# Kernel optimization log

Measured on AMD Instinct MI355X. Metric: run time of the kernel, lower is better.

Reference implementation:

```python
import jax, jax.numpy as jnp
import numpy as np

N_NODES = 100000


def gcn_conv(x, src, dst, W, b):
    # PyG GCNConv: add self-loops, symmetric norm D^-1/2 (A+I) D^-1/2, then linear.
    n = x.shape[0]
    xw = x @ W  # [N, out]
    deg = jax.ops.segment_sum(jnp.ones_like(dst, dtype=xw.dtype), dst, num_segments=n)
    dinv = jnp.where(deg > 0, jax.lax.rsqrt(deg), 0.0)
    norm = dinv[src] * dinv[dst]  # [E_total]
    out = jax.ops.segment_sum(norm[:, None] * xw[src], dst, num_segments=n)
    return out + b


def setup_inputs() -> dict:
    key = jax.random.key(0)
    k1, k2, k3, k4, k5, k6 = jax.random.split(key, 6)
    d = 64
    E = 1600000
    x = jax.random.normal(k1, (N_NODES, d), dtype=jnp.float32)
    edge_index = jax.random.randint(k2, (2, E), 0, N_NODES, dtype=jnp.int64)
    s = 1.0 / np.sqrt(d)
    W1 = jax.random.normal(k3, (d, d), dtype=jnp.float32) * s
    b1 = jax.random.normal(k4, (d,), dtype=jnp.float32) * 0.01
    W2 = jax.random.normal(k5, (d, d), dtype=jnp.float32) * s
    b2 = jax.random.normal(k6, (d,), dtype=jnp.float32) * 0.01
    return {"x": x, "edge_index": edge_index, "W1": W1, "b1": b1, "W2": W2, "b2": b2}


def reference(x, edge_index, W1, b1, W2, b2):
    n = x.shape[0]
    loops = jnp.arange(n, dtype=edge_index.dtype)
    src = jnp.concatenate([edge_index[0], loops])
    dst = jnp.concatenate([edge_index[1], loops])
    out = jax.nn.relu(gcn_conv(x, src, dst, W1, b1))
    out = gcn_conv(out, src, dst, W2, b2)
    return jax.nn.relu(out + x)
```

## Files before the change

kernel.cpp:

```cpp
#include <hip/hip_runtime.h>

constexpr int BIN_CHUNK = 2048;
constexpr int BK_SHIFT  = 8;
constexpr int BK_NODES  = 1 << BK_SHIFT;
constexpr int NBMAX     = 512;
constexpr int CAP       = 5120;

typedef short bf16x8 __attribute__((ext_vector_type(8)));
typedef float f32x4 __attribute__((ext_vector_type(4)));

static __device__ __forceinline__ float4 mkf4(float x, float y, float z, float w) {
  float4 r; r.x = x; r.y = y; r.z = z; r.w = w; return r;
}

static __device__ __forceinline__ unsigned short bf16rne(float f) {
  unsigned u = __float_as_uint(f);
  u = (u + 0x7fffu + ((u >> 16) & 1u)) >> 16;
  return (unsigned short)u;
}
static __device__ __forceinline__ unsigned pack_bf16(float a, float b) {
  return (unsigned)bf16rne(a) | ((unsigned)bf16rne(b) << 16);
}
static __device__ __forceinline__ float blo(unsigned v) { return __uint_as_float(v << 16); }
static __device__ __forceinline__ float bhi(unsigned v) { return __uint_as_float(v & 0xffff0000u); }


__global__ void k_zero(int* __restrict__ p) { p[threadIdx.x] = 0; }


__global__ __launch_bounds__(256) void k_bin(const int* __restrict__ src,
                                             const int* __restrict__ dst,
                                             int* __restrict__ bcur,
                                             int* __restrict__ binned, int E) {
  __shared__ int lh[4][NBMAX];
  __shared__ int cbase[4][NBMAX];
  const int tid = threadIdx.x, wv = tid >> 6, lane = tid & 63;
  for (int i = lane; i < NBMAX; i += 64) lh[wv][i] = 0;
  __syncthreads();

  const int e0 = blockIdx.x * BIN_CHUNK;
  const int e1 = min(e0 + BIN_CHUNK, E);
  const int q  = BIN_CHUNK / 4;
  const int we0 = min(e0 + wv * q, e1);
  const int we1 = min(we0 + q, e1);
  const bool vec = (we1 - we0 == q) &&
                   (((((size_t)(dst + we0)) | ((size_t)(src + we0))) & 15) == 0);

  if (vec) {
    const int4* __restrict__ d4 = (const int4*)(dst + we0);
#pragma unroll
    for (int j = 0; j < 2; ++j) {
      int4 d = d4[lane + j * 64];
      atomicAdd(&lh[wv][d.x >> BK_SHIFT], 1);
      atomicAdd(&lh[wv][d.y >> BK_SHIFT], 1);
      atomicAdd(&lh[wv][d.z >> BK_SHIFT], 1);
      atomicAdd(&lh[wv][d.w >> BK_SHIFT], 1);
    }
  } else {
    for (int e = we0 + lane; e < we1; e += 64)
      atomicAdd(&lh[wv][dst[e] >> BK_SHIFT], 1);
  }
  __syncthreads();

  for (int b = tid; b < NBMAX; b += 256) {
    int c0 = lh[0][b], c1 = lh[1][b], c2 = lh[2][b], c3 = lh[3][b];
    int tot = c0 + c1 + c2 + c3;
    int base = tot ? atomicAdd(bcur + b, tot) : 0;
    cbase[0][b] = base;
    cbase[1][b] = base + c0;
    cbase[2][b] = base + c0 + c1;
    cbase[3][b] = base + c0 + c1 + c2;
    lh[0][b] = 0; lh[1][b] = 0; lh[2][b] = 0; lh[3][b] = 0;
  }
  __syncthreads();

  if (vec) {
    const int4* __restrict__ d4 = (const int4*)(dst + we0);
    const int4* __restrict__ s4 = (const int4*)(src + we0);
#pragma unroll
    for (int j = 0; j < 2; ++j) {
      int4 d = d4[lane + j * 64];
      int4 s = s4[lane + j * 64];
      int b, pos;
      b = d.x >> BK_SHIFT; pos = cbase[wv][b] + atomicAdd(&lh[wv][b], 1);
      if (pos < CAP) binned[b * CAP + pos] = s.x | ((d.x & (BK_NODES - 1)) << 17);
      b = d.y >> BK_SHIFT; pos = cbase[wv][b] + atomicAdd(&lh[wv][b], 1);
      if (pos < CAP) binned[b * CAP + pos] = s.y | ((d.y & (BK_NODES - 1)) << 17);
      b = d.z >> BK_SHIFT; pos = cbase[wv][b] + atomicAdd(&lh[wv][b], 1);
      if (pos < CAP) binned[b * CAP + pos] = s.z | ((d.z & (BK_NODES - 1)) << 17);
      b = d.w >> BK_SHIFT; pos = cbase[wv][b] + atomicAdd(&lh[wv][b], 1);
      if (pos < CAP) binned[b * CAP + pos] = s.w | ((d.w & (BK_NODES - 1)) << 17);
    }
  } else {
    for (int e = we0 + lane; e < we1; e += 64) {
      int d = dst[e];
      int b = d >> BK_SHIFT;
      int pos = cbase[wv][b] + atomicAdd(&lh[wv][b], 1);
      if (pos < CAP) binned[b * CAP + pos] = src[e] | ((d & (BK_NODES - 1)) << 17);
    }
  }
}


__global__ __launch_bounds__(256) void k_place3(const int* __restrict__ bcur,
                                                const int* __restrict__ binned,
                                                int2* __restrict__ nfo,
                                                float* __restrict__ dinv,
                                                int* __restrict__ col, int N) {
  __shared__ int lhw[4][BK_NODES];
  __shared__ int lplace[CAP];
  __shared__ int wsum[4];
  const int tid = threadIdx.x, lane = tid & 63, wv = tid >> 6;
  const int b = blockIdx.x;
  const int nb0 = b << BK_SHIFT;
  const int base = b * CAP;
  const int len = min(bcur[b], CAP);

#pragma unroll
  for (int i = 0; i < 4; ++i) ((int*)lhw)[tid + i * 256] = 0;
  __syncthreads();

  const int q = (len + 3) >> 2;
  const int we0 = min(wv * q, len);
  const int we1 = min(we0 + q, len);

  for (int e = we0 + lane; e < we1; e += 64)
    atomicAdd(&lhw[wv][binned[base + e] >> 17], 1);
  __syncthreads();

  const int c = lhw[0][tid] + lhw[1][tid] + lhw[2][tid] + lhw[3][tid];
  int t = c;
#pragma unroll
  for (int o = 1; o < 64; o <<= 1) { int n = __shfl_up(t, o); if (lane >= o) t += n; }
  if (lane == 63) wsum[wv] = t;
  __syncthreads();
  int wbase = 0;
#pragma unroll
  for (int w = 0; w < 3; ++w) if (w < wv) wbase += wsum[w];
  const int excl = wbase + t - c;

  const int node = nb0 + tid;
  if (node < N) {
    int2 s; s.x = base + excl; s.y = base + excl + c;
    nfo[node] = s;
    dinv[node] = rsqrtf((float)(c + 1));
  }

  int run = excl;
#pragma unroll
  for (int w = 0; w < 4; ++w) { int tmp = lhw[w][tid]; lhw[w][tid] = run; run += tmp; }
  __syncthreads();

  for (int e = we0 + lane; e < we1; e += 64) {
    int v = binned[base + e];
    int pos = atomicAdd(&lhw[wv][v >> 17], 1);
    lplace[pos] = v & 0x1FFFF;
  }
  __syncthreads();

  const int n4 = len >> 2;
  int4* __restrict__ c4 = (int4*)(col + base);
  const int4* __restrict__ p4 = (const int4*)lplace;
  for (int i = tid; i < n4; i += 256) c4[i] = p4[i];
  for (int e = (n4 << 2) + tid; e < len; e += 256) col[base + e] = lplace[e];
}



__global__ __launch_bounds__(256) void k_gemmf(const float* __restrict__ X,
                                               const float* __restrict__ W,
                                               const float* __restrict__ dinv,
                                               unsigned short* __restrict__ Y, int N) {
  __shared__ float Wl[4096];
  const int tid = threadIdx.x;
  {
    const float4* __restrict__ W4 = (const float4*)W;
    float4* __restrict__ Wl4 = (float4*)Wl;
#pragma unroll
    for (int i = 0; i < 4; ++i) Wl4[tid + i * 256] = W4[tid + i * 256];
  }
  __syncthreads();

  const int lane = tid & 63, wave = tid >> 6;
  const int g = lane >> 4, r = lane & 15;
  const int row0 = blockIdx.x * 64 + wave * 16;

  bf16x8 Bf[4][2];
#pragma unroll
  for (int t = 0; t < 4; ++t)
#pragma unroll
    for (int s = 0; s < 2; ++s) {
      const int kb = s * 32 + g * 8;
      const int cc = t * 16 + r;
#pragma unroll
      for (int j = 0; j < 8; ++j)
        Bf[t][s][j] = (short)bf16rne(Wl[(kb + j) * 64 + cc]);
    }

  const int arow = min(row0 + r, N - 1);
  bf16x8 Af[2];
#pragma unroll
  for (int s = 0; s < 2; ++s) {
    const float4 x0 = *(const float4*)(X + (size_t)arow * 64 + s * 32 + g * 8);
    const float4 x1 = *(const float4*)(X + (size_t)arow * 64 + s * 32 + g * 8 + 4);
    Af[s][0] = (short)bf16rne(x0.x); Af[s][1] = (short)bf16rne(x0.y);
    Af[s][2] = (short)bf16rne(x0.z); Af[s][3] = (short)bf16rne(x0.w);
    Af[s][4] = (short)bf16rne(x1.x); Af[s][5] = (short)bf16rne(x1.y);
    Af[s][6] = (short)bf16rne(x1.z); Af[s][7] = (short)bf16rne(x1.w);
  }

  f32x4 acc[4];
#pragma unroll
  for (int t = 0; t < 4; ++t) acc[t] = (f32x4)0.f;
#pragma unroll
  for (int t = 0; t < 4; ++t) {
    acc[t] = __builtin_amdgcn_mfma_f32_16x16x32_bf16(Af[0], Bf[t][0], acc[t], 0, 0, 0);
    acc[t] = __builtin_amdgcn_mfma_f32_16x16x32_bf16(Af[1], Bf[t][1], acc[t], 0, 0, 0);
  }

#pragma unroll
  for (int b = 0; b < 4; ++b) {
    const int row = row0 + g * 4 + b;
    if (row < N) {
      const float di = dinv[row];
#pragma unroll
      for (int t = 0; t < 4; ++t)
        Y[(size_t)row * 64 + t * 16 + r] = bf16rne(di * acc[t][b]);
    }
  }
}


__global__ __launch_bounds__(256) void k_gemmb(const unsigned* __restrict__ H,
                                               const float* __restrict__ W,
                                               const float* __restrict__ dinv,
                                               unsigned short* __restrict__ Y, int N) {
  __shared__ float Wl[4096];
  const int tid = threadIdx.x;
  {
    const float4* __restrict__ W4 = (const float4*)W;
    float4* __restrict__ Wl4 = (float4*)Wl;
#pragma unroll
    for (int i = 0; i < 4; ++i) Wl4[tid + i * 256] = W4[tid + i * 256];
  }
  __syncthreads();

  const int lane = tid & 63, wave = tid >> 6;
  const int g = lane >> 4, r = lane & 15;
  const int row0 = blockIdx.x * 64 + wave * 16;

  bf16x8 Bf[4][2];
#pragma unroll
  for (int t = 0; t < 4; ++t)
#pragma unroll
    for (int s = 0; s < 2; ++s) {
      const int kb = s * 32 + g * 8;
      const int cc = t * 16 + r;
#pragma unroll
      for (int j = 0; j < 8; ++j)
        Bf[t][s][j] = (short)bf16rne(Wl[(kb + j) * 64 + cc]);
    }

  const int arow = min(row0 + r, N - 1);
  bf16x8 Af[2];
#pragma unroll
  for (int s = 0; s < 2; ++s) {
    uint4 hv = *(const uint4*)(H + (size_t)arow * 32 + s * 16 + g * 4);
    Af[s] = *(const bf16x8*)&hv;
  }

  f32x4 acc[4];
#pragma unroll
  for (int t = 0; t < 4; ++t) acc[t] = (f32x4)0.f;
#pragma unroll
  for (int t = 0; t < 4; ++t) {
    acc[t] = __builtin_amdgcn_mfma_f32_16x16x32_bf16(Af[0], Bf[t][0], acc[t], 0, 0, 0);
    acc[t] = __builtin_amdgcn_mfma_f32_16x16x32_bf16(Af[1], Bf[t][1], acc[t], 0, 0, 0);
  }

#pragma unroll
  for (int b = 0; b < 4; ++b) {
    const int row = row0 + g * 4 + b;
    if (row < N) {
      const float di = dinv[row];
#pragma unroll
      for (int t = 0; t < 4; ++t)
        Y[(size_t)row * 64 + t * 16 + r] = bf16rne(di * acc[t][b]);
    }
  }
}


template <int MODE>
__global__ __launch_bounds__(256) void k_gather(const int2* __restrict__ nfo,
                                                const int* __restrict__ col,
                                                const float* __restrict__ dinv,
                                                const uint2* __restrict__ xws2,
                                                const float4* __restrict__ b4,
                                                const float4* __restrict__ x4,
                                                void* __restrict__ outp, int N) {
  const int node = blockIdx.x * 4 + (threadIdx.x >> 6);
  if (node >= N) return;
  const int lane = threadIdx.x & 63;
  const int sub = lane >> 4;
  const int lg = lane & 15;

  const int2 se = nfo[node];
  const uint2 sv = xws2[(size_t)node * 16 + lg];
  const float di = dinv[node];
  const float4 bb = b4[lg];
  float4 xx = mkf4(0.f, 0.f, 0.f, 0.f);
  if (MODE == 2) xx = x4[(size_t)node * 16 + lg];

  const int s0 = se.x;
  const int deg = se.y - se.x;
  const int dcap = min(deg, 64);

  int cv = 0;
  if (deg > 0) cv = col[min(s0 + lane, s0 + deg - 1)];

  float a0 = 0.f, a1 = 0.f, a2 = 0.f, a3 = 0.f;

  int jb = 0;
  for (; jb + 16 <= dcap; jb += 16) {
    int c0 = __shfl(cv, jb + sub);
    int c1 = __shfl(cv, jb + 4 + sub);
    int c2 = __shfl(cv, jb + 8 + sub);
    int c3 = __shfl(cv, jb + 12 + sub);
    uint2 v0 = xws2[(size_t)c0 * 16 + lg];
    uint2 v1 = xws2[(size_t)c1 * 16 + lg];
    uint2 v2 = xws2[(size_t)c2 * 16 + lg];
    uint2 v3 = xws2[(size_t)c3 * 16 + lg];
    a0 += (blo(v0.x) + blo(v1.x)) + (blo(v2.x) + blo(v3.x));
    a1 += (bhi(v0.x) + bhi(v1.x)) + (bhi(v2.x) + bhi(v3.x));
    a2 += (blo(v0.y) + blo(v1.y)) + (blo(v2.y) + blo(v3.y));
    a3 += (bhi(v0.y) + bhi(v1.y)) + (bhi(v2.y) + bhi(v3.y));
  }
  if (jb < dcap) {
    const int j0 = jb + sub, j1 = jb + 4 + sub, j2 = jb + 8 + sub, j3 = jb + 12 + sub;
    const int m = dcap - 1;
    int c0 = __shfl(cv, min(j0, m));
    int c1 = __shfl(cv, min(j1, m));
    int c2 = __shfl(cv, min(j2, m));
    int c3 = __shfl(cv, min(j3, m));
    uint2 v0 = xws2[(size_t)c0 * 16 + lg];
    uint2 v1 = xws2[(size_t)c1 * 16 + lg];
    uint2 v2 = xws2[(size_t)c2 * 16 + lg];
    uint2 v3 = xws2[(size_t)c3 * 16 + lg];
    a0 += (j0 < dcap ? blo(v0.x) : 0.f) + (j1 < dcap ? blo(v1.x) : 0.f)
        + (j2 < dcap ? blo(v2.x) : 0.f) + (j3 < dcap ? blo(v3.x) : 0.f);
    a1 += (j0 < dcap ? bhi(v0.x) : 0.f) + (j1 < dcap ? bhi(v1.x) : 0.f)
        + (j2 < dcap ? bhi(v2.x) : 0.f) + (j3 < dcap ? bhi(v3.x) : 0.f);
    a2 += (j0 < dcap ? blo(v0.y) : 0.f) + (j1 < dcap ? blo(v1.y) : 0.f)
        + (j2 < dcap ? blo(v2.y) : 0.f) + (j3 < dcap ? blo(v3.y) : 0.f);
    a3 += (j0 < dcap ? bhi(v0.y) : 0.f) + (j1 < dcap ? bhi(v1.y) : 0.f)
        + (j2 < dcap ? bhi(v2.y) : 0.f) + (j3 < dcap ? bhi(v3.y) : 0.f);
  }
  for (int e = s0 + 64 + sub; e < s0 + deg; e += 4) {
    uint2 v = xws2[(size_t)col[e] * 16 + lg];
    a0 += blo(v.x); a1 += bhi(v.x); a2 += blo(v.y); a3 += bhi(v.y);
  }

  a0 += __shfl_xor(a0, 16); a1 += __shfl_xor(a1, 16);
  a2 += __shfl_xor(a2, 16); a3 += __shfl_xor(a3, 16);
  a0 += __shfl_xor(a0, 32); a1 += __shfl_xor(a1, 32);
  a2 += __shfl_xor(a2, 32); a3 += __shfl_xor(a3, 32);

  if (sub == 0) {
    a0 += blo(sv.x); a1 += bhi(sv.x); a2 += blo(sv.y); a3 += bhi(sv.y);
    float r0 = fmaf(di, a0, bb.x);
    float r1 = fmaf(di, a1, bb.y);
    float r2 = fmaf(di, a2, bb.z);
    float r3 = fmaf(di, a3, bb.w);
    if (MODE == 2) {
      r0 += xx.x; r1 += xx.y; r2 += xx.z; r3 += xx.w;
      ((float4*)outp)[(size_t)node * 16 + lg] =
          mkf4(fmaxf(r0, 0.f), fmaxf(r1, 0.f), fmaxf(r2, 0.f), fmaxf(r3, 0.f));
    } else {
      uint2 o;
      o.x = pack_bf16(fmaxf(r0, 0.f), fmaxf(r1, 0.f));
      o.y = pack_bf16(fmaxf(r2, 0.f), fmaxf(r3, 0.f));
      ((uint2*)outp)[(size_t)node * 16 + lg] = o;
    }
  }
}


extern "C" void kernel_launch(void* const* d_in, const int* in_sizes, int n_in,
                              void* d_out, int out_size, void* d_ws, size_t ws_size,
                              hipStream_t stream) {
  const float* x  = (const float*)d_in[0];
  const int*   ei = (const int*)d_in[1];
  const float* W1 = (const float*)d_in[2];
  const float* b1 = (const float*)d_in[3];
  const float* W2 = (const float*)d_in[4];
  const float* b2 = (const float*)d_in[5];
  float* out = (float*)d_out;

  const int N = in_sizes[0] / 64;
  const int E = in_sizes[1] / 2;
  const int NB = (N + BK_NODES - 1) >> BK_SHIFT;

  const int* srcp = ei;
  const int* dstp = ei + E;

  auto align = [](size_t v) { return (v + 255) & ~(size_t)255; };
  char* ws = (char*)d_ws;
  size_t o = 0;
  int2* nfo   = (int2*)(ws + o); o = align(o + (size_t)N * 8);
  float* dinv = (float*)(ws + o); o = align(o + (size_t)N * 4);
  int* bcur   = (int*)(ws + o); o = align(o + NBMAX * 4);
  int* col    = (int*)(ws + o); o = align(o + (size_t)NB * CAP * 4);
  unsigned* xws = (unsigned*)(ws + o); o = align(o + (size_t)N * 128);
  unsigned* h1  = (unsigned*)(ws + o); o = align(o + (size_t)N * 128);
  int* binned = (int*)h1;

  const int bGm  = (N + 63) / 64;
  const int bG   = (N + 3) / 4;
  const int bBin = (E + BIN_CHUNK - 1) / BIN_CHUNK;

  k_zero<<<1, NBMAX, 0, stream>>>(bcur);
  k_bin<<<bBin, 256, 0, stream>>>(srcp, dstp, bcur, binned, E);
  k_place3<<<NB, 256, 0, stream>>>(bcur, binned, nfo, dinv, col, N);

  k_gemmf<<<bGm, 256, 0, stream>>>(x, W1, dinv, (unsigned short*)xws, N);
  k_gather<1><<<bG, 256, 0, stream>>>(nfo, col, dinv, (const uint2*)xws,
                                      (const float4*)b1, (const float4*)x,
                                      (void*)h1, N);

  k_gemmb<<<bGm, 256, 0, stream>>>(h1, W2, dinv, (unsigned short*)xws, N);
  k_gather<2><<<bG, 256, 0, stream>>>(nfo, col, dinv, (const uint2*)xws,
                                      (const float4*)b2, (const float4*)x,
                                      (void*)out, N);
}
```

Before: 148.0 us.

## Fuse zero, bin, and place stages into one cooperative kernel with grid syncs

Merges the bcur zeroing, edge binning and per-bucket placement kernels into a single cooperative launch that separates phases with grid-wide syncs and loops blocks over chunks and buckets. The aim is to cut two kernel launches and their inter-kernel gaps. It also hardcodes 256 CUs when sizing the grid, adds the cost of grid barriers, and reduces occupancy because of the union shared-memory footprint. The old three-kernel path is kept as a fallback if the cooperative launch fails.

```diff
diff --git a/kernel.cpp b/kernel.cpp
--- a/kernel.cpp
+++ b/kernel.cpp
@@ -1,4 +1,7 @@
 #include <hip/hip_runtime.h>
+#include <hip/hip_cooperative_groups.h>
+
+namespace cg = cooperative_groups;
 
 constexpr int BIN_CHUNK = 2048;
 constexpr int BK_SHIFT  = 8;
@@ -25,20 +28,20 @@
 static __device__ __forceinline__ float bhi(unsigned v) { return __uint_as_float(v & 0xffff0000u); }
 
 
-__global__ void k_zero(int* __restrict__ p) { p[threadIdx.x] = 0; }
-
-
-__global__ __launch_bounds__(256) void k_bin(const int* __restrict__ src,
-                                             const int* __restrict__ dst,
-                                             int* __restrict__ bcur,
-                                             int* __restrict__ binned, int E) {
-  __shared__ int lh[4][NBMAX];
-  __shared__ int cbase[4][NBMAX];
+struct BinSmem { int lh[4][NBMAX]; int cbase[4][NBMAX]; };
+struct PlaceSmem { int lhw[4][BK_NODES]; int lplace[CAP]; int wsum[4]; };
+
+static __device__ __forceinline__ void bin_body(BinSmem& sm,
+                                                const int* __restrict__ src,
+                                                const int* __restrict__ dst,
+                                                int* __restrict__ bcur,
+                                                int* __restrict__ binned,
+                                                int E, int NB, int chunk) {
   const int tid = threadIdx.x, wv = tid >> 6, lane = tid & 63;
-  for (int i = lane; i < NBMAX; i += 64) lh[wv][i] = 0;
-  __syncthreads();
-
-  const int e0 = blockIdx.x * BIN_CHUNK;
+  for (int i = lane; i < NBMAX; i += 64) sm.lh[wv][i] = 0;
+  __syncthreads();
+
+  const int e0 = chunk * BIN_CHUNK;
   const int e1 = min(e0 + BIN_CHUNK, E);
   const int q  = BIN_CHUNK / 4;
   const int we0 = min(e0 + wv * q, e1);
@@ -51,26 +54,26 @@
 #pragma unroll
     for (int j = 0; j < 2; ++j) {
       int4 d = d4[lane + j * 64];
-      atomicAdd(&lh[wv][d.x >> BK_SHIFT], 1);
-      atomicAdd(&lh[wv][d.y >> BK_SHIFT], 1);
-      atomicAdd(&lh[wv][d.z >> BK_SHIFT], 1);
-      atomicAdd(&lh[wv][d.w >> BK_SHIFT], 1);
+      atomicAdd(&sm.lh[wv][d.x >> BK_SHIFT], 1);
+      atomicAdd(&sm.lh[wv][d.y >> BK_SHIFT], 1);
+      atomicAdd(&sm.lh[wv][d.z >> BK_SHIFT], 1);
+      atomicAdd(&sm.lh[wv][d.w >> BK_SHIFT], 1);
     }
   } else {
     for (int e = we0 + lane; e < we1; e += 64)
-      atomicAdd(&lh[wv][dst[e] >> BK_SHIFT], 1);
-  }
-  __syncthreads();
-
-  for (int b = tid; b < NBMAX; b += 256) {
-    int c0 = lh[0][b], c1 = lh[1][b], c2 = lh[2][b], c3 = lh[3][b];
+      atomicAdd(&sm.lh[wv][dst[e] >> BK_SHIFT], 1);
+  }
+  __syncthreads();
+
+  for (int b = tid; b < NB; b += 256) {
+    int c0 = sm.lh[0][b], c1 = sm.lh[1][b], c2 = sm.lh[2][b], c3 = sm.lh[3][b];
     int tot = c0 + c1 + c2 + c3;
     int base = tot ? atomicAdd(bcur + b, tot) : 0;
-    cbase[0][b] = base;
-    cbase[1][b] = base + c0;
-    cbase[2][b] = base + c0 + c1;
-    cbase[3][b] = base + c0 + c1 + c2;
-    lh[0][b] = 0; lh[1][b] = 0; lh[2][b] = 0; lh[3][b] = 0;
+    sm.cbase[0][b] = base;
+    sm.cbase[1][b] = base + c0;
+    sm.cbase[2][b] = base + c0 + c1;
+    sm.cbase[3][b] = base + c0 + c1 + c2;
+    sm.lh[0][b] = 0; sm.lh[1][b] = 0; sm.lh[2][b] = 0; sm.lh[3][b] = 0;
   }
   __syncthreads();
 
@@ -82,89 +85,133 @@
       int4 d = d4[lane + j * 64];
       int4 s = s4[lane + j * 64];
       int b, pos;
-      b = d.x >> BK_SHIFT; pos = cbase[wv][b] + atomicAdd(&lh[wv][b], 1);
+      b = d.x >> BK_SHIFT; pos = sm.cbase[wv][b] + atomicAdd(&sm.lh[wv][b], 1);
       if (pos < CAP) binned[b * CAP + pos] = s.x | ((d.x & (BK_NODES - 1)) << 17);
-      b = d.y >> BK_SHIFT; pos = cbase[wv][b] + atomicAdd(&lh[wv][b], 1);
+      b = d.y >> BK_SHIFT; pos = sm.cbase[wv][b] + atomicAdd(&sm.lh[wv][b], 1);
       if (pos < CAP) binned[b * CAP + pos] = s.y | ((d.y & (BK_NODES - 1)) << 17);
-      b = d.z >> BK_SHIFT; pos = cbase[wv][b] + atomicAdd(&lh[wv][b], 1);
+      b = d.z >> BK_SHIFT; pos = sm.cbase[wv][b] + atomicAdd(&sm.lh[wv][b], 1);
       if (pos < CAP) binned[b * CAP + pos] = s.z | ((d.z & (BK_NODES - 1)) << 17);
-      b = d.w >> BK_SHIFT; pos = cbase[wv][b] + atomicAdd(&lh[wv][b], 1);
+      b = d.w >> BK_SHIFT; pos = sm.cbase[wv][b] + atomicAdd(&sm.lh[wv][b], 1);
       if (pos < CAP) binned[b * CAP + pos] = s.w | ((d.w & (BK_NODES - 1)) << 17);
     }
   } else {
     for (int e = we0 + lane; e < we1; e += 64) {
       int d = dst[e];
       int b = d >> BK_SHIFT;
-      int pos = cbase[wv][b] + atomicAdd(&lh[wv][b], 1);
+      int pos = sm.cbase[wv][b] + atomicAdd(&sm.lh[wv][b], 1);
       if (pos < CAP) binned[b * CAP + pos] = src[e] | ((d & (BK_NODES - 1)) << 17);
     }
   }
-}
-
+  __syncthreads();
+}
+
+static __device__ __forceinline__ void place_body(PlaceSmem& sm,
+                                                  const int* __restrict__ bcur,
+                                                  const int* __restrict__ binned,
+                                                  int2* __restrict__ nfo,
+                                                  float* __restrict__ dinv,
+                                                  int* __restrict__ col,
+                                                  int N, int b) {
+  const int tid = threadIdx.x, lane = tid & 63, wv = tid >> 6;
+  const int nb0 = b << BK_SHIFT;
+  const int base = b * CAP;
+  const int len = min(bcur[b], CAP);
+
+#pragma unroll
+  for (int i = 0; i < 4; ++i) ((int*)sm.lhw)[tid + i * 256] = 0;
+  __syncthreads();
+
+  const int q = (len + 3) >> 2;
+  const int we0 = min(wv * q, len);
+  const int we1 = min(we0 + q, len);
+
+  for (int e = we0 + lane; e < we1; e += 64)
+    atomicAdd(&sm.lhw[wv][binned[base + e] >> 17], 1);
+  __syncthreads();
+
+  const int c = sm.lhw[0][tid] + sm.lhw[1][tid] + sm.lhw[2][tid] + sm.lhw[3][tid];
+  int t = c;
+#pragma unroll
+  for (int o = 1; o < 64; o <<= 1) { int n = __shfl_up(t, o); if (lane >= o) t += n; }
+  if (lane == 63) sm.wsum[wv] = t;
+  __syncthreads();
+  int wbase = 0;
+#pragma unroll
+  for (int w = 0; w < 3; ++w) if (w < wv) wbase += sm.wsum[w];
+  const int excl = wbase + t - c;
+
+  const int node = nb0 + tid;
+  if (node < N) {
+    int2 s; s.x = base + excl; s.y = base + excl + c;
+    nfo[node] = s;
+    dinv[node] = rsqrtf((float)(c + 1));
+  }
+
+  int run = excl;
+#pragma unroll
+  for (int w = 0; w < 4; ++w) { int tmp = sm.lhw[w][tid]; sm.lhw[w][tid] = run; run += tmp; }
+  __syncthreads();
+
+  for (int e = we0 + lane; e < we1; e += 64) {
+    int v = binned[base + e];
+    int pos = atomicAdd(&sm.lhw[wv][v >> 17], 1);
+    sm.lplace[pos] = v & 0x1FFFF;
+  }
+  __syncthreads();
+
+  const int n4 = len >> 2;
+  int4* __restrict__ c4 = (int4*)(col + base);
+  const int4* __restrict__ p4 = (const int4*)sm.lplace;
+  for (int i = tid; i < n4; i += 256) c4[i] = p4[i];
+  for (int e = (n4 << 2) + tid; e < len; e += 256) col[base + e] = sm.lplace[e];
+  __syncthreads();
+}
+
+
+__global__ __launch_bounds__(256) void k_build(const int* __restrict__ src,
+                                               const int* __restrict__ dst,
+                                               int* __restrict__ bcur,
+                                               int* __restrict__ binned,
+                                               int2* __restrict__ nfo,
+                                               float* __restrict__ dinv,
+                                               int* __restrict__ col,
+                                               int N, int E, int NB,
+                                               int nChunks, int G) {
+  __shared__ union { BinSmem b; PlaceSmem p; } sm;
+  cg::grid_group grid = cg::this_grid();
+
+  if (blockIdx.x == 0)
+    for (int i = threadIdx.x; i < NBMAX; i += 256) bcur[i] = 0;
+  grid.sync();
+
+  for (int chunk = blockIdx.x; chunk < nChunks; chunk += G)
+    bin_body(sm.b, src, dst, bcur, binned, E, NB, chunk);
+  grid.sync();
+
+  for (int b = blockIdx.x; b < NB; b += G)
+    place_body(sm.p, bcur, binned, nfo, dinv, col, N, b);
+}
+
+
+__global__ void k_zero(int* __restrict__ p) { p[threadIdx.x] = 0; }
+
+__global__ __launch_bounds__(256) void k_bin(const int* __restrict__ src,
+                                             const int* __restrict__ dst,
+                                             int* __restrict__ bcur,
+                                             int* __restrict__ binned,
+                                             int E, int NB) {
+  __shared__ BinSmem sm;
+  bin_body(sm, src, dst, bcur, binned, E, NB, blockIdx.x);
+}
 
 __global__ __launch_bounds__(256) void k_place3(const int* __restrict__ bcur,
                                                 const int* __restrict__ binned,
                                                 int2* __restrict__ nfo,
                                                 float* __restrict__ dinv,
                                                 int* __restrict__ col, int N) {
-  __shared__ int lhw[4][BK_NODES];
-  __shared__ int lplace[CAP];
-  __shared__ int wsum[4];
-  const int tid = threadIdx.x, lane = tid & 63, wv = tid >> 6;
-  const int b = blockIdx.x;
-  const int nb0 = b << BK_SHIFT;
-  const int base = b * CAP;
-  const int len = min(bcur[b], CAP);
-
-#pragma unroll
-  for (int i = 0; i < 4; ++i) ((int*)lhw)[tid + i * 256] = 0;
-  __syncthreads();
-
-  const int q = (len + 3) >> 2;
-  const int we0 = min(wv * q, len);
-  const int we1 = min(we0 + q, len);
-
-  for (int e = we0 + lane; e < we1; e += 64)
-    atomicAdd(&lhw[wv][binned[base + e] >> 17], 1);
-  __syncthreads();
-
-  const int c = lhw[0][tid] + lhw[1][tid] + lhw[2][tid] + lhw[3][tid];
-  int t = c;
-#pragma unroll
-  for (int o = 1; o < 64; o <<= 1) { int n = __shfl_up(t, o); if (lane >= o) t += n; }
-  if (lane == 63) wsum[wv] = t;
-  __syncthreads();
-  int wbase = 0;
-#pragma unroll
-  for (int w = 0; w < 3; ++w) if (w < wv) wbase += wsum[w];
-  const int excl = wbase + t - c;
-
-  const int node = nb0 + tid;
-  if (node < N) {
-    int2 s; s.x = base + excl; s.y = base + excl + c;
-    nfo[node] = s;
-    dinv[node] = rsqrtf((float)(c + 1));
-  }
-
-  int run = excl;
-#pragma unroll
-  for (int w = 0; w < 4; ++w) { int tmp = lhw[w][tid]; lhw[w][tid] = run; run += tmp; }
-  __syncthreads();
-
-  for (int e = we0 + lane; e < we1; e += 64) {
-    int v = binned[base + e];
-    int pos = atomicAdd(&lhw[wv][v >> 17], 1);
-    lplace[pos] = v & 0x1FFFF;
-  }
-  __syncthreads();
-
-  const int n4 = len >> 2;
-  int4* __restrict__ c4 = (int4*)(col + base);
-  const int4* __restrict__ p4 = (const int4*)lplace;
-  for (int i = tid; i < n4; i += 256) c4[i] = p4[i];
-  for (int e = (n4 << 2) + tid; e < len; e += 256) col[base + e] = lplace[e];
-}
-
+  __shared__ PlaceSmem sm;
+  place_body(sm, bcur, binned, nfo, dinv, col, N, blockIdx.x);
+}
 
 
 __global__ __launch_bounds__(256) void k_gemmf(const float* __restrict__ X,
@@ -229,7 +276,6 @@
     }
   }
 }
-
 
 __global__ __launch_bounds__(256) void k_gemmb(const unsigned* __restrict__ H,
                                                const float* __restrict__ W,
@@ -399,7 +445,7 @@
 
   const int N = in_sizes[0] / 64;
   const int E = in_sizes[1] / 2;
-  const int NB = (N + BK_NODES - 1) >> BK_SHIFT;
+  int NB = (N + BK_NODES - 1) >> BK_SHIFT;
 
   const int* srcp = ei;
   const int* dstp = ei + E;
@@ -417,11 +463,28 @@
 
   const int bGm  = (N + 63) / 64;
   const int bG   = (N + 3) / 4;
-  const int bBin = (E + BIN_CHUNK - 1) / BIN_CHUNK;
-
-  k_zero<<<1, NBMAX, 0, stream>>>(bcur);
-  k_bin<<<bBin, 256, 0, stream>>>(srcp, dstp, bcur, binned, E);
-  k_place3<<<NB, 256, 0, stream>>>(bcur, binned, nfo, dinv, col, N);
+  int bBin = (E + BIN_CHUNK - 1) / BIN_CHUNK;
+
+  bool coop_done = false;
+  {
+    int maxBpc = 0;
+    if (hipOccupancyMaxActiveBlocksPerMultiprocessor(&maxBpc, k_build, 256, 0)
+            == hipSuccess && maxBpc > 0) {
+      int G = maxBpc * 256;
+      if (G > bBin) G = bBin;
+      void* args[] = {(void*)&srcp, (void*)&dstp, (void*)&bcur, (void*)&binned,
+                      (void*)&nfo, (void*)&dinv, (void*)&col,
+                      (void*)&N, (void*)&E, (void*)&NB, (void*)&bBin, (void*)&G};
+      if (hipLaunchCooperativeKernel((void*)k_build, dim3(G), dim3(256),
+                                     args, 0, stream) == hipSuccess)
+        coop_done = true;
+    }
+  }
+  if (!coop_done) {
+    k_zero<<<1, NBMAX, 0, stream>>>(bcur);
+    k_bin<<<bBin, 256, 0, stream>>>(srcp, dstp, bcur, binned, E, NB);
+    k_place3<<<NB, 256, 0, stream>>>(bcur, binned, nfo, dinv, col, N);
+  }
 
   k_gemmf<<<bGm, 256, 0, stream>>>(x, W1, dinv, (unsigned short*)xws, N);
   k_gather<1><<<bG, 256, 0, stream>>>(nfo, col, dinv, (const uint2*)xws,
```

Measured after the change: 298.6 us. 2.02x slower.
